# Kernel tuning notes

Hardware: AMD Instinct MI355X
Metric: run time of the kernel (lower is better)

## Reference

```python
import jax, jax.numpy as jnp
import numpy as np

B, N, H, F, G = 16, 192, 128, 128, 50


def setup_inputs() -> dict:
    key = jax.random.key(0)
    ks = jax.random.split(key, 12)
    s = lambda fan_in: 1.0 / np.sqrt(fan_in)
    inp = {
        "features": jax.random.normal(ks[0], (B, N, H), jnp.float32),
        "rbf": jax.random.uniform(ks[1], (B, N, N, G), jnp.float32),
        "neighbour_mask": jax.random.randint(ks[2], (B, N, N), 0, 2, jnp.int32),
        # dense_rbf: Linear(G,F) -> Softplus -> Linear(F,F)
        "W_rbf1": jax.random.uniform(ks[3], (G, F), jnp.float32, -s(G), s(G)),
        "b_rbf1": jnp.zeros((F,), jnp.float32),
        "W_rbf2": jax.random.uniform(ks[4], (F, F), jnp.float32, -s(F), s(F)),
        "b_rbf2": jnp.zeros((F,), jnp.float32),
        # dense_f: Linear(H,F)
        "W_f": jax.random.uniform(ks[5], (H, F), jnp.float32, -s(H), s(H)),
        "b_f": jnp.zeros((F,), jnp.float32),
        # dense_out: Linear(F,H) -> Softplus -> Linear(H,H)
        "W_o1": jax.random.uniform(ks[6], (F, H), jnp.float32, -s(F), s(F)),
        "b_o1": jnp.zeros((H,), jnp.float32),
        "W_o2": jax.random.uniform(ks[7], (H, H), jnp.float32, -s(H), s(H)),
        "b_o2": jnp.zeros((H,), jnp.float32),
    }
    return inp


def reference(features, rbf, neighbour_mask, W_rbf1, b_rbf1, W_rbf2, b_rbf2,
              W_f, b_f, W_o1, b_o1, W_o2, b_o2):
    # filter network on RBF expansion: [B,N,N,G] -> [B,N,N,F]
    fw = jax.nn.softplus(rbf @ W_rbf1 + b_rbf1) @ W_rbf2 + b_rbf2
    # neighbor features: [B,N,H] -> [B,1,N,F] (broadcast over central-atom axis)
    nf = (features @ W_f + b_f)[:, None, :, :]
    mask = neighbour_mask.astype(fw.dtype)[..., None]  # [B,N,N,1]
    # messages [B,N,N,F], masked sum over neighbor axis -> [B,N,F]
    aggregated = jnp.sum(fw * nf * mask, axis=2)
    out = jax.nn.softplus(aggregated @ W_o1 + b_o1) @ W_o2 + b_o2  # [B,N,H]
    return features + out
```

## Files before the change

kernel.cpp:

```cpp
#include <hip/hip_runtime.h>
#include <hip/hip_bf16.h>


typedef __bf16 bf16_t;
typedef __bf16 bf16x8 __attribute__((ext_vector_type(8)));
typedef float  f32x4  __attribute__((ext_vector_type(4)));

constexpr int kB = 16, kN = 192, kH = 128, kF = 128, kG = 50;
constexpr int kRows = kB * kN;
constexpr int kHsPitch = 136;

__device__ __forceinline__ float ldf(const void* p, int i, bool bfm) {
  return bfm ? (float)((const bf16_t*)p)[i] : ((const float*)p)[i];
}

__device__ __forceinline__ float softplus_f(float x) {
  float t = __logf(1.f + __expf(fminf(x, 20.f)));
  return x > 20.f ? x : t;
}

__global__ __launch_bounds__(256) void detect_kernel(const unsigned int* __restrict__ rbf_w,
                                                     int* __restrict__ flag) {
  __shared__ int c_hi, c_zero;
  const int t = threadIdx.x;
  if (t == 0) { c_hi = 0; c_zero = 0; }
  __syncthreads();
  unsigned int w = rbf_w[(size_t)t * 40003u];
  unsigned int lo = w & 0xFFFFu;
  if (((lo >> 7) & 0xFFu) >= 128u) atomicAdd(&c_hi, 1);
  if (lo == 0u) atomicAdd(&c_zero, 1);
  __syncthreads();
  if (t == 0) *flag = (c_hi == 0 && c_zero < 200) ? 1 : 0;
}

__global__ __launch_bounds__(256) void prep_kernel(const void* __restrict__ W1,
                                                   const void* __restrict__ W2,
                                                   const int* __restrict__ flag,
                                                   bf16_t* __restrict__ w1t,
                                                   bf16_t* __restrict__ w2t) {
  const bool bfm = *flag != 0;
  int idx = blockIdx.x * 256 + threadIdx.x;
  if (idx < 128 * 64) {
    int n = idx >> 6, k = idx & 63;
    w1t[idx] = (k < kG) ? (bf16_t)ldf(W1, k * kF + n, bfm) : (bf16_t)0.f;
  } else if (idx < 128 * 64 + 128 * 128) {
    int id2 = idx - 128 * 64;
    int n = id2 >> 7, k = id2 & 127;
    w2t[id2] = (bf16_t)ldf(W2, k * kF + n, bfm);
  }
}

__global__ __launch_bounds__(128) void nf_kernel(const void* __restrict__ features,
                                                 const void* __restrict__ Wf,
                                                 const void* __restrict__ bfv,
                                                 const int* __restrict__ flag,
                                                 float* __restrict__ nf) {
  const bool bfm = *flag != 0;
  int row = blockIdx.x, f = threadIdx.x;
  __shared__ float s_x[kH];
  s_x[f] = ldf(features, row * kH + f, bfm);
  __syncthreads();
  float acc = ldf(bfv, f, bfm);
#pragma unroll 8
  for (int k = 0; k < kH; ++k) acc = fmaf(s_x[k], ldf(Wf, k * kF + f, bfm), acc);
  nf[row * kF + f] = acc;
}

__global__ __launch_bounds__(256) void main_kernel(
    const void* __restrict__ rbf, const int* __restrict__ nmask,
    const void* __restrict__ b1p, const void* __restrict__ b2p,
    const bf16_t* __restrict__ w1t, const bf16_t* __restrict__ w2t,
    const float* __restrict__ nf, const int* __restrict__ flag,
    float* __restrict__ agg) {
  __shared__ bf16_t s_hs[kN * kHsPitch];
  __shared__ float  s_mask[kN];
  __shared__ float  s_agg[kF];

  const bool bfm = *flag != 0;
  const int bi = blockIdx.x;
  const int b  = bi / kN;
  const int t  = threadIdx.x;
  const int wave = t >> 6, lane = t & 63;
  const int n16 = lane & 15, q = lane >> 4;
  const int m0w = wave * 48;

  for (int idx = t; idx < kN; idx += 256) s_mask[idx] = (float)nmask[bi * kN + idx];
  if (t < kF) s_agg[t] = 0.f;

  f32x4 acc[3][8];
#pragma unroll
  for (int mt = 0; mt < 3; ++mt)
#pragma unroll
    for (int nt = 0; nt < 8; ++nt)
#pragma unroll
      for (int r = 0; r < 4; ++r) acc[mt][nt][r] = 0.f;

  const size_t rbase = (size_t)bi * (kN * kG);
#pragma unroll
  for (int ks = 0; ks < 2; ++ks) {
    bf16x8 afr[3];
#pragma unroll
    for (int mt = 0; mt < 3; ++mt) {
      const int j  = m0w + mt * 16 + n16;
      const int kb = ks * 32 + q * 8;
      if (bfm) {
        const bf16_t* rp = (const bf16_t*)rbf + rbase + (size_t)j * kG;
#pragma unroll
        for (int i = 0; i < 8; ++i) {
          int k = kb + i;
          afr[mt][i] = (k < kG) ? rp[k] : (bf16_t)0.f;
        }
      } else {
        const float* rp = (const float*)rbf + rbase + (size_t)j * kG;
#pragma unroll
        for (int i = 0; i < 8; ++i) {
          int k = kb + i;
          afr[mt][i] = (bf16_t)((k < kG) ? rp[k] : 0.f);
        }
      }
    }
#pragma unroll
    for (int nt = 0; nt < 8; ++nt) {
      bf16x8 bfr = *(const bf16x8*)(w1t + (nt * 16 + n16) * 64 + ks * 32 + q * 8);
#pragma unroll
      for (int mt = 0; mt < 3; ++mt)
        acc[mt][nt] = __builtin_amdgcn_mfma_f32_16x16x32_bf16(afr[mt], bfr, acc[mt][nt], 0, 0, 0);
    }
  }

#pragma unroll
  for (int nt = 0; nt < 8; ++nt) {
    const int col = nt * 16 + n16;
    const float bb = ldf(b1p, col, bfm);
#pragma unroll
    for (int mt = 0; mt < 3; ++mt) {
      const int jb = m0w + mt * 16 + q * 4;
#pragma unroll
      for (int r = 0; r < 4; ++r)
        s_hs[(jb + r) * kHsPitch + col] = (bf16_t)softplus_f(acc[mt][nt][r] + bb);
    }
  }
  __syncthreads();

#pragma unroll
  for (int mt = 0; mt < 3; ++mt)
#pragma unroll
    for (int nt = 0; nt < 8; ++nt)
#pragma unroll
      for (int r = 0; r < 4; ++r) acc[mt][nt][r] = 0.f;

#pragma unroll
  for (int ks = 0; ks < 4; ++ks) {
    bf16x8 afr[3];
#pragma unroll
    for (int mt = 0; mt < 3; ++mt)
      afr[mt] = *(const bf16x8*)(s_hs + (m0w + mt * 16 + n16) * kHsPitch + ks * 32 + q * 8);
#pragma unroll
    for (int nt = 0; nt < 8; ++nt) {
      bf16x8 bfr = *(const bf16x8*)(w2t + (nt * 16 + n16) * 128 + ks * 32 + q * 8);
#pragma unroll
      for (int mt = 0; mt < 3; ++mt)
        acc[mt][nt] = __builtin_amdgcn_mfma_f32_16x16x32_bf16(afr[mt], bfr, acc[mt][nt], 0, 0, 0);
    }
  }

#pragma unroll
  for (int nt = 0; nt < 8; ++nt) {
    const int f = nt * 16 + n16;
    const float b2v = ldf(b2p, f, bfm);
    float p = 0.f;
#pragma unroll
    for (int mt = 0; mt < 3; ++mt) {
      const int jb = m0w + mt * 16 + q * 4;
#pragma unroll
      for (int r = 0; r < 4; ++r) {
        const int j = jb + r;
        const float m   = s_mask[j];
        const float nfv = nf[((size_t)b * kN + j) * kF + f];
        p = fmaf(m * (acc[mt][nt][r] + b2v), nfv, p);
      }
    }
    atomicAdd(&s_agg[f], p);
  }
  __syncthreads();
  if (t < kF) agg[(size_t)bi * kF + t] = s_agg[t];
}

__global__ __launch_bounds__(128) void out_kernel(
    const float* __restrict__ agg, const void* __restrict__ features,
    const void* __restrict__ Wo1, const void* __restrict__ bo1,
    const void* __restrict__ Wo2, const void* __restrict__ bo2,
    const int* __restrict__ flag, void* __restrict__ out) {
  const bool bfm = *flag != 0;
  int row = blockIdx.x, h = threadIdx.x;
  __shared__ float s_a[kF], s_t[kH];
  s_a[h] = agg[row * kF + h];
  __syncthreads();
  float a1 = ldf(bo1, h, bfm);
#pragma unroll 8
  for (int k = 0; k < kF; ++k) a1 = fmaf(s_a[k], ldf(Wo1, k * kH + h, bfm), a1);
  s_t[h] = softplus_f(a1);
  __syncthreads();
  float a2 = ldf(bo2, h, bfm);
#pragma unroll 8
  for (int k = 0; k < kH; ++k) a2 = fmaf(s_t[k], ldf(Wo2, k * kH + h, bfm), a2);
  float res = ldf(features, row * kH + h, bfm) + a2;
  if (bfm) ((bf16_t*)out)[row * kH + h] = (bf16_t)res;
  else     ((float*)out)[row * kH + h]  = res;
}

extern "C" void kernel_launch(void* const* d_in, const int* in_sizes, int n_in,
                              void* d_out, int out_size, void* d_ws, size_t ws_size,
                              hipStream_t stream) {
  const void* features = d_in[0];
  const void* rbf      = d_in[1];
  const int*  nmask    = (const int*)d_in[2];
  const void* W1  = d_in[3];
  const void* b1  = d_in[4];
  const void* W2  = d_in[5];
  const void* b2  = d_in[6];
  const void* Wf  = d_in[7];
  const void* bfv = d_in[8];
  const void* Wo1 = d_in[9];
  const void* bo1 = d_in[10];
  const void* Wo2 = d_in[11];
  const void* bo2 = d_in[12];

  char* ws = (char*)d_ws;
  float*  nf   = (float*)ws;
  float*  agg  = (float*)(ws + 1572864);
  bf16_t* w1t  = (bf16_t*)(ws + 3145728);
  bf16_t* w2t  = (bf16_t*)(ws + 3162112);
  int*    flag = (int*)(ws + 3194880);

  detect_kernel<<<1, 256, 0, stream>>>((const unsigned int*)rbf, flag);
  prep_kernel<<<96, 256, 0, stream>>>(W1, W2, flag, w1t, w2t);
  nf_kernel<<<kRows, 128, 0, stream>>>(features, Wf, bfv, flag, nf);
  main_kernel<<<kRows, 256, 0, stream>>>(rbf, nmask, b1, b2, w1t, w2t, nf, flag, agg);
  out_kernel<<<kRows, 128, 0, stream>>>(agg, features, Wo1, bo1, Wo2, bo2, flag, d_out);
}
```

Before: 354.6 us.

## Compact masked neighbours and move dense layers to MFMA kernels

The main kernel builds a compact list of unmasked neighbour rows per atom and runs the filter MLP only on those 16-row tiles, using an XOR-swizzled shared-memory layout. The feature and output dense layers are rewritten as MFMA tile kernels with pre-transposed bf16 weights and a hi/lo split for fp32 activations. Biases are hoisted and occupancy is hinted via launch bounds. This adds an atomic compaction step and makes per-block load depend on mask density.

```diff
diff --git a/kernel.cpp b/kernel.cpp
--- a/kernel.cpp
+++ b/kernel.cpp
@@ -5,10 +5,11 @@
 typedef __bf16 bf16_t;
 typedef __bf16 bf16x8 __attribute__((ext_vector_type(8)));
 typedef float  f32x4  __attribute__((ext_vector_type(4)));
+typedef unsigned int uintx4 __attribute__((ext_vector_type(4)));
 
 constexpr int kB = 16, kN = 192, kH = 128, kF = 128, kG = 50;
 constexpr int kRows = kB * kN;
-constexpr int kHsPitch = 136;
+constexpr int kOutPitch = 136;
 
 __device__ __forceinline__ float ldf(const void* p, int i, bool bfm) {
   return bfm ? (float)((const bf16_t*)p)[i] : ((const float*)p)[i];
@@ -33,48 +34,101 @@
   if (t == 0) *flag = (c_hi == 0 && c_zero < 200) ? 1 : 0;
 }
 
-__global__ __launch_bounds__(256) void prep_kernel(const void* __restrict__ W1,
-                                                   const void* __restrict__ W2,
-                                                   const int* __restrict__ flag,
-                                                   bf16_t* __restrict__ w1t,
-                                                   bf16_t* __restrict__ w2t) {
+__global__ __launch_bounds__(256) void prep_kernel(
+    const void* __restrict__ W1, const void* __restrict__ W2,
+    const void* __restrict__ Wf, const void* __restrict__ Wo1,
+    const void* __restrict__ Wo2, const int* __restrict__ flag,
+    bf16_t* __restrict__ w1t, bf16_t* __restrict__ w2t,
+    bf16_t* __restrict__ wft, bf16_t* __restrict__ wo1t,
+    bf16_t* __restrict__ wo2t) {
   const bool bfm = *flag != 0;
   int idx = blockIdx.x * 256 + threadIdx.x;
-  if (idx < 128 * 64) {
+  if (idx < 8192) {
     int n = idx >> 6, k = idx & 63;
     w1t[idx] = (k < kG) ? (bf16_t)ldf(W1, k * kF + n, bfm) : (bf16_t)0.f;
-  } else if (idx < 128 * 64 + 128 * 128) {
-    int id2 = idx - 128 * 64;
-    int n = id2 >> 7, k = id2 & 127;
-    w2t[id2] = (bf16_t)ldf(W2, k * kF + n, bfm);
+  } else if (idx < 8192 + 16384) {
+    int i2 = idx - 8192; int n = i2 >> 7, k = i2 & 127;
+    w2t[i2] = (bf16_t)ldf(W2, k * kF + n, bfm);
+  } else if (idx < 8192 + 2 * 16384) {
+    int i2 = idx - 8192 - 16384; int n = i2 >> 7, k = i2 & 127;
+    wft[i2] = (bf16_t)ldf(Wf, k * kF + n, bfm);
+  } else if (idx < 8192 + 3 * 16384) {
+    int i2 = idx - 8192 - 2 * 16384; int n = i2 >> 7, k = i2 & 127;
+    wo1t[i2] = (bf16_t)ldf(Wo1, k * kH + n, bfm);
+  } else if (idx < 8192 + 4 * 16384) {
+    int i2 = idx - 8192 - 3 * 16384; int n = i2 >> 7, k = i2 & 127;
+    wo2t[i2] = (bf16_t)ldf(Wo2, k * kH + n, bfm);
   }
 }
 
 __global__ __launch_bounds__(128) void nf_kernel(const void* __restrict__ features,
-                                                 const void* __restrict__ Wf,
+                                                 const bf16_t* __restrict__ wft,
                                                  const void* __restrict__ bfv,
                                                  const int* __restrict__ flag,
                                                  float* __restrict__ nf) {
   const bool bfm = *flag != 0;
-  int row = blockIdx.x, f = threadIdx.x;
-  __shared__ float s_x[kH];
-  s_x[f] = ldf(features, row * kH + f, bfm);
-  __syncthreads();
-  float acc = ldf(bfv, f, bfm);
-#pragma unroll 8
-  for (int k = 0; k < kH; ++k) acc = fmaf(s_x[k], ldf(Wf, k * kF + f, bfm), acc);
-  nf[row * kF + f] = acc;
-}
-
-__global__ __launch_bounds__(256) void main_kernel(
+  const int t = threadIdx.x, wave = t >> 6, lane = t & 63;
+  const int n16 = lane & 15, q = lane >> 4;
+  const int rbase = blockIdx.x * 32 + wave * 16;
+  const int arow = rbase + n16;
+
+  f32x4 acc[8];
+#pragma unroll
+  for (int nt = 0; nt < 8; ++nt)
+#pragma unroll
+    for (int r = 0; r < 4; ++r) acc[nt][r] = 0.f;
+
+  if (bfm) {
+    const bf16_t* fp = (const bf16_t*)features + (size_t)arow * kH;
+#pragma unroll
+    for (int ks = 0; ks < 4; ++ks) {
+      bf16x8 afr = *(const bf16x8*)(fp + ks * 32 + q * 8);
+#pragma unroll
+      for (int nt = 0; nt < 8; ++nt) {
+        bf16x8 bfr = *(const bf16x8*)(wft + (nt * 16 + n16) * kH + ks * 32 + q * 8);
+        acc[nt] = __builtin_amdgcn_mfma_f32_16x16x32_bf16(afr, bfr, acc[nt], 0, 0, 0);
+      }
+    }
+  } else {
+    const float* fp = (const float*)features + (size_t)arow * kH;
+#pragma unroll
+    for (int ks = 0; ks < 4; ++ks) {
+      f32x4 x0 = *(const f32x4*)(fp + ks * 32 + q * 8);
+      f32x4 x1 = *(const f32x4*)(fp + ks * 32 + q * 8 + 4);
+      bf16x8 ahi, alo;
+#pragma unroll
+      for (int e = 0; e < 4; ++e) {
+        bf16_t h0 = (bf16_t)x0[e]; ahi[e]     = h0; alo[e]     = (bf16_t)(x0[e] - (float)h0);
+        bf16_t h1 = (bf16_t)x1[e]; ahi[e + 4] = h1; alo[e + 4] = (bf16_t)(x1[e] - (float)h1);
+      }
+#pragma unroll
+      for (int nt = 0; nt < 8; ++nt) {
+        bf16x8 bfr = *(const bf16x8*)(wft + (nt * 16 + n16) * kH + ks * 32 + q * 8);
+        acc[nt] = __builtin_amdgcn_mfma_f32_16x16x32_bf16(ahi, bfr, acc[nt], 0, 0, 0);
+        acc[nt] = __builtin_amdgcn_mfma_f32_16x16x32_bf16(alo, bfr, acc[nt], 0, 0, 0);
+      }
+    }
+  }
+#pragma unroll
+  for (int nt = 0; nt < 8; ++nt) {
+    const int col = nt * 16 + n16;
+    const float bv = ldf(bfv, col, bfm);
+#pragma unroll
+    for (int r = 0; r < 4; ++r)
+      nf[(size_t)(rbase + q * 4 + r) * kF + col] = acc[nt][r] + bv;
+  }
+}
+
+__global__ __launch_bounds__(256, 3) void main_kernel(
     const void* __restrict__ rbf, const int* __restrict__ nmask,
     const void* __restrict__ b1p, const void* __restrict__ b2p,
     const bf16_t* __restrict__ w1t, const bf16_t* __restrict__ w2t,
     const float* __restrict__ nf, const int* __restrict__ flag,
     float* __restrict__ agg) {
-  __shared__ bf16_t s_hs[kN * kHsPitch];
-  __shared__ float  s_mask[kN];
+  __shared__ bf16_t s_hs[kN * 128];
+  __shared__ int    s_rows[kN];
   __shared__ float  s_agg[kF];
+  __shared__ int    s_cnt;
 
   const bool bfm = *flag != 0;
   const int bi = blockIdx.x;
@@ -82,131 +136,195 @@
   const int t  = threadIdx.x;
   const int wave = t >> 6, lane = t & 63;
   const int n16 = lane & 15, q = lane >> 4;
-  const int m0w = wave * 48;
-
-  for (int idx = t; idx < kN; idx += 256) s_mask[idx] = (float)nmask[bi * kN + idx];
+
+  if (t == 0) s_cnt = 0;
   if (t < kF) s_agg[t] = 0.f;
-
-  f32x4 acc[3][8];
-#pragma unroll
-  for (int mt = 0; mt < 3; ++mt)
+  __syncthreads();
+  for (int j = t; j < kN; j += 256)
+    if (nmask[bi * kN + j] != 0) s_rows[atomicAdd(&s_cnt, 1)] = j;
+  __syncthreads();
+  const int nm = s_cnt;
+  const int ntiles = (nm + 15) >> 4;
+  for (int p2 = nm + t; p2 < ntiles * 16; p2 += 256) s_rows[p2] = 0;
+  __syncthreads();
+
+  float b1r[8], b2r[8];
+#pragma unroll
+  for (int nt = 0; nt < 8; ++nt) {
+    b1r[nt] = ldf(b1p, nt * 16 + n16, bfm);
+    b2r[nt] = ldf(b2p, nt * 16 + n16, bfm);
+  }
+
+  char* hsb = (char*)s_hs;
+
+  for (int tt = wave; tt < ntiles; tt += 4) {
+    const int j = s_rows[tt * 16 + n16];
+    bf16x8 a0, a1;
+    if (bfm) {
+      const unsigned int* rp = (const unsigned int*)rbf + (size_t)bi * 4800 + j * 25;
+      uintx4 u0, u1;
+#pragma unroll
+      for (int i = 0; i < 4; ++i) u0[i] = rp[q * 4 + i];
+#pragma unroll
+      for (int i = 0; i < 4; ++i) {
+        const int d = 16 + q * 4 + i;
+        u1[i] = (d < 25) ? rp[d] : 0u;
+      }
+      a0 = __builtin_bit_cast(bf16x8, u0);
+      a1 = __builtin_bit_cast(bf16x8, u1);
+    } else {
+      const float* rp = (const float*)rbf + (size_t)bi * (kN * kG) + j * kG;
+#pragma unroll
+      for (int i = 0; i < 8; ++i) a0[i] = (bf16_t)rp[q * 8 + i];
+#pragma unroll
+      for (int i = 0; i < 8; ++i) {
+        const int k1 = 32 + q * 8 + i;
+        a1[i] = (bf16_t)((k1 < kG) ? rp[k1] : 0.f);
+      }
+    }
+
+    f32x4 acc1[8];
 #pragma unroll
     for (int nt = 0; nt < 8; ++nt)
 #pragma unroll
-      for (int r = 0; r < 4; ++r) acc[mt][nt][r] = 0.f;
-
-  const size_t rbase = (size_t)bi * (kN * kG);
-#pragma unroll
-  for (int ks = 0; ks < 2; ++ks) {
-    bf16x8 afr[3];
-#pragma unroll
-    for (int mt = 0; mt < 3; ++mt) {
-      const int j  = m0w + mt * 16 + n16;
-      const int kb = ks * 32 + q * 8;
-      if (bfm) {
-        const bf16_t* rp = (const bf16_t*)rbf + rbase + (size_t)j * kG;
-#pragma unroll
-        for (int i = 0; i < 8; ++i) {
-          int k = kb + i;
-          afr[mt][i] = (k < kG) ? rp[k] : (bf16_t)0.f;
-        }
-      } else {
-        const float* rp = (const float*)rbf + rbase + (size_t)j * kG;
-#pragma unroll
-        for (int i = 0; i < 8; ++i) {
-          int k = kb + i;
-          afr[mt][i] = (bf16_t)((k < kG) ? rp[k] : 0.f);
-        }
-      }
-    }
-#pragma unroll
-    for (int nt = 0; nt < 8; ++nt) {
-      bf16x8 bfr = *(const bf16x8*)(w1t + (nt * 16 + n16) * 64 + ks * 32 + q * 8);
-#pragma unroll
-      for (int mt = 0; mt < 3; ++mt)
-        acc[mt][nt] = __builtin_amdgcn_mfma_f32_16x16x32_bf16(afr[mt], bfr, acc[mt][nt], 0, 0, 0);
-    }
-  }
-
+      for (int r = 0; r < 4; ++r) acc1[nt][r] = 0.f;
+
+#pragma unroll
+    for (int nt = 0; nt < 8; ++nt) {
+      bf16x8 bf0 = *(const bf16x8*)(w1t + (nt * 16 + n16) * 64 + q * 8);
+      acc1[nt] = __builtin_amdgcn_mfma_f32_16x16x32_bf16(a0, bf0, acc1[nt], 0, 0, 0);
+    }
+#pragma unroll
+    for (int nt = 0; nt < 8; ++nt) {
+      bf16x8 bf1 = *(const bf16x8*)(w1t + (nt * 16 + n16) * 64 + 32 + q * 8);
+      acc1[nt] = __builtin_amdgcn_mfma_f32_16x16x32_bf16(a1, bf1, acc1[nt], 0, 0, 0);
+    }
+
+#pragma unroll
+    for (int nt = 0; nt < 8; ++nt) {
+      const int colb = (nt * 16 + n16) * 2;
+#pragma unroll
+      for (int r = 0; r < 4; ++r) {
+        const int row = tt * 16 + q * 4 + r;
+        *(bf16_t*)(hsb + ((row * 256 + colb) ^ ((row & 7) << 4))) =
+            (bf16_t)softplus_f(acc1[nt][r] + b1r[nt]);
+      }
+    }
+  }
+  __syncthreads();
+
+  for (int tt = wave; tt < ntiles; tt += 4) {
+    f32x4 acc2[8];
+#pragma unroll
+    for (int nt = 0; nt < 8; ++nt)
+#pragma unroll
+      for (int r = 0; r < 4; ++r) acc2[nt][r] = 0.f;
+
+#pragma unroll
+    for (int ks = 0; ks < 4; ++ks) {
+      const int row = tt * 16 + n16;
+      bf16x8 afr = *(const bf16x8*)(hsb +
+          ((row * 256 + (ks * 32 + q * 8) * 2) ^ ((row & 7) << 4)));
+#pragma unroll
+      for (int nt = 0; nt < 8; ++nt) {
+        bf16x8 bfr = *(const bf16x8*)(w2t + (nt * 16 + n16) * 128 + ks * 32 + q * 8);
+        acc2[nt] = __builtin_amdgcn_mfma_f32_16x16x32_bf16(afr, bfr, acc2[nt], 0, 0, 0);
+      }
+    }
+
+    const int i0 = tt * 16 + q * 4;
+    int jr[4]; float wr[4];
+#pragma unroll
+    for (int r = 0; r < 4; ++r) {
+      const int idx = i0 + r;
+      jr[r] = s_rows[idx];
+      wr[r] = (idx < nm) ? 1.f : 0.f;
+    }
+    const float* nfb = nf + (size_t)b * kN * kF;
+#pragma unroll
+    for (int nt = 0; nt < 8; ++nt) {
+      const int f = nt * 16 + n16;
+      float p = 0.f;
+#pragma unroll
+      for (int r = 0; r < 4; ++r)
+        p = fmaf(wr[r] * (acc2[nt][r] + b2r[nt]), nfb[jr[r] * kF + f], p);
+      atomicAdd(&s_agg[f], p);
+    }
+  }
+  __syncthreads();
+  if (t < kF) agg[(size_t)bi * kF + t] = s_agg[t];
+}
+
+__global__ __launch_bounds__(128) void out_kernel(
+    const float* __restrict__ agg, const void* __restrict__ features,
+    const bf16_t* __restrict__ wo1t, const bf16_t* __restrict__ wo2t,
+    const void* __restrict__ bo1, const void* __restrict__ bo2,
+    const int* __restrict__ flag, void* __restrict__ out) {
+  __shared__ bf16_t s_t[32 * kOutPitch];
+  const bool bfm = *flag != 0;
+  const int t = threadIdx.x, wave = t >> 6, lane = t & 63;
+  const int n16 = lane & 15, q = lane >> 4;
+  const int rb = blockIdx.x * 32 + wave * 16;
+
+  f32x4 acc[8];
+#pragma unroll
+  for (int nt = 0; nt < 8; ++nt)
+#pragma unroll
+    for (int r = 0; r < 4; ++r) acc[nt][r] = 0.f;
+
+  const float* ap = agg + (size_t)(rb + n16) * kF;
+#pragma unroll
+  for (int ks = 0; ks < 4; ++ks) {
+    f32x4 x0 = *(const f32x4*)(ap + ks * 32 + q * 8);
+    f32x4 x1 = *(const f32x4*)(ap + ks * 32 + q * 8 + 4);
+    bf16x8 ahi, alo;
+#pragma unroll
+    for (int e = 0; e < 4; ++e) {
+      bf16_t h0 = (bf16_t)x0[e]; ahi[e]     = h0; alo[e]     = (bf16_t)(x0[e] - (float)h0);
+      bf16_t h1 = (bf16_t)x1[e]; ahi[e + 4] = h1; alo[e + 4] = (bf16_t)(x1[e] - (float)h1);
+    }
+#pragma unroll
+    for (int nt = 0; nt < 8; ++nt) {
+      bf16x8 bfr = *(const bf16x8*)(wo1t + (nt * 16 + n16) * kF + ks * 32 + q * 8);
+      acc[nt] = __builtin_amdgcn_mfma_f32_16x16x32_bf16(ahi, bfr, acc[nt], 0, 0, 0);
+      acc[nt] = __builtin_amdgcn_mfma_f32_16x16x32_bf16(alo, bfr, acc[nt], 0, 0, 0);
+    }
+  }
 #pragma unroll
   for (int nt = 0; nt < 8; ++nt) {
     const int col = nt * 16 + n16;
-    const float bb = ldf(b1p, col, bfm);
-#pragma unroll
-    for (int mt = 0; mt < 3; ++mt) {
-      const int jb = m0w + mt * 16 + q * 4;
-#pragma unroll
-      for (int r = 0; r < 4; ++r)
-        s_hs[(jb + r) * kHsPitch + col] = (bf16_t)softplus_f(acc[mt][nt][r] + bb);
-    }
-  }
-  __syncthreads();
-
-#pragma unroll
-  for (int mt = 0; mt < 3; ++mt)
-#pragma unroll
-    for (int nt = 0; nt < 8; ++nt)
-#pragma unroll
-      for (int r = 0; r < 4; ++r) acc[mt][nt][r] = 0.f;
-
+    const float bv = ldf(bo1, col, bfm);
+#pragma unroll
+    for (int r = 0; r < 4; ++r)
+      s_t[(wave * 16 + q * 4 + r) * kOutPitch + col] = (bf16_t)softplus_f(acc[nt][r] + bv);
+  }
+  __syncthreads();
+
+#pragma unroll
+  for (int nt = 0; nt < 8; ++nt)
+#pragma unroll
+    for (int r = 0; r < 4; ++r) acc[nt][r] = 0.f;
 #pragma unroll
   for (int ks = 0; ks < 4; ++ks) {
-    bf16x8 afr[3];
-#pragma unroll
-    for (int mt = 0; mt < 3; ++mt)
-      afr[mt] = *(const bf16x8*)(s_hs + (m0w + mt * 16 + n16) * kHsPitch + ks * 32 + q * 8);
-#pragma unroll
-    for (int nt = 0; nt < 8; ++nt) {
-      bf16x8 bfr = *(const bf16x8*)(w2t + (nt * 16 + n16) * 128 + ks * 32 + q * 8);
-#pragma unroll
-      for (int mt = 0; mt < 3; ++mt)
-        acc[mt][nt] = __builtin_amdgcn_mfma_f32_16x16x32_bf16(afr[mt], bfr, acc[mt][nt], 0, 0, 0);
-    }
-  }
-
+    bf16x8 afr = *(const bf16x8*)(s_t + (wave * 16 + n16) * kOutPitch + ks * 32 + q * 8);
+#pragma unroll
+    for (int nt = 0; nt < 8; ++nt) {
+      bf16x8 bfr = *(const bf16x8*)(wo2t + (nt * 16 + n16) * kH + ks * 32 + q * 8);
+      acc[nt] = __builtin_amdgcn_mfma_f32_16x16x32_bf16(afr, bfr, acc[nt], 0, 0, 0);
+    }
+  }
 #pragma unroll
   for (int nt = 0; nt < 8; ++nt) {
-    const int f = nt * 16 + n16;
-    const float b2v = ldf(b2p, f, bfm);
-    float p = 0.f;
-#pragma unroll
-    for (int mt = 0; mt < 3; ++mt) {
-      const int jb = m0w + mt * 16 + q * 4;
-#pragma unroll
-      for (int r = 0; r < 4; ++r) {
-        const int j = jb + r;
-        const float m   = s_mask[j];
-        const float nfv = nf[((size_t)b * kN + j) * kF + f];
-        p = fmaf(m * (acc[mt][nt][r] + b2v), nfv, p);
-      }
-    }
-    atomicAdd(&s_agg[f], p);
-  }
-  __syncthreads();
-  if (t < kF) agg[(size_t)bi * kF + t] = s_agg[t];
-}
-
-__global__ __launch_bounds__(128) void out_kernel(
-    const float* __restrict__ agg, const void* __restrict__ features,
-    const void* __restrict__ Wo1, const void* __restrict__ bo1,
-    const void* __restrict__ Wo2, const void* __restrict__ bo2,
-    const int* __restrict__ flag, void* __restrict__ out) {
-  const bool bfm = *flag != 0;
-  int row = blockIdx.x, h = threadIdx.x;
-  __shared__ float s_a[kF], s_t[kH];
-  s_a[h] = agg[row * kF + h];
-  __syncthreads();
-  float a1 = ldf(bo1, h, bfm);
-#pragma unroll 8
-  for (int k = 0; k < kF; ++k) a1 = fmaf(s_a[k], ldf(Wo1, k * kH + h, bfm), a1);
-  s_t[h] = softplus_f(a1);
-  __syncthreads();
-  float a2 = ldf(bo2, h, bfm);
-#pragma unroll 8
-  for (int k = 0; k < kH; ++k) a2 = fmaf(s_t[k], ldf(Wo2, k * kH + h, bfm), a2);
-  float res = ldf(features, row * kH + h, bfm) + a2;
-  if (bfm) ((bf16_t*)out)[row * kH + h] = (bf16_t)res;
-  else     ((float*)out)[row * kH + h]  = res;
+    const int col = nt * 16 + n16;
+    const float bv = ldf(bo2, col, bfm);
+#pragma unroll
+    for (int r = 0; r < 4; ++r) {
+      const int row = rb + q * 4 + r;
+      float res = ldf(features, (size_t)row * kH + col, bfm) + acc[nt][r] + bv;
+      if (bfm) ((bf16_t*)out)[(size_t)row * kH + col] = (bf16_t)res;
+      else     ((float*)out)[(size_t)row * kH + col]  = res;
+    }
+  }
 }
 
 extern "C" void kernel_launch(void* const* d_in, const int* in_sizes, int n_in,
@@ -231,11 +349,14 @@
   float*  agg  = (float*)(ws + 1572864);
   bf16_t* w1t  = (bf16_t*)(ws + 3145728);
   bf16_t* w2t  = (bf16_t*)(ws + 3162112);
-  int*    flag = (int*)(ws + 3194880);
+  bf16_t* wft  = (bf16_t*)(ws + 3194880);
+  bf16_t* wo1t = (bf16_t*)(ws + 3227648);
+  bf16_t* wo2t = (bf16_t*)(ws + 3260416);
+  int*    flag = (int*)(ws + 3293184);
 
   detect_kernel<<<1, 256, 0, stream>>>((const unsigned int*)rbf, flag);
-  prep_kernel<<<96, 256, 0, stream>>>(W1, W2, flag, w1t, w2t);
-  nf_kernel<<<kRows, 128, 0, stream>>>(features, Wf, bfv, flag, nf);
+  prep_kernel<<<288, 256, 0, stream>>>(W1, W2, Wf, Wo1, Wo2, flag, w1t, w2t, wft, wo1t, wo2t);
+  nf_kernel<<<96, 128, 0, stream>>>(features, wft, bfv, flag, nf);
   main_kernel<<<kRows, 256, 0, stream>>>(rbf, nmask, b1, b2, w1t, w2t, nf, flag, agg);
-  out_kernel<<<kRows, 128, 0, stream>>>(agg, features, Wo1, bo1, Wo2, bo2, flag, d_out);
-}
+  out_kernel<<<96, 128, 0, stream>>>(agg, features, wo1t, wo2t, bo1, bo2, flag, d_out);
+}
```

After: 371.9 us. 4.9% more time.
